# Performance work log

Measured on AMD Instinct MI355X. Metric: run time of the kernel, lower is better.

The kernel has to match this reference:

```python
import jax, jax.numpy as jnp
import numpy as np

B, N, L, E = 8, 2000, 128, 2048  # batch, nodes, local_size+1, ff_hidden_dim
PENALTY = 10.0


def setup_inputs() -> dict:
    key = jax.random.key(0)
    ks = jax.random.split(key, 8)
    dist = jax.random.uniform(ks[0], (B, N, N), jnp.float32) + 1e-3  # positive distances
    theta = jax.random.normal(ks[1], (B, N, N), jnp.float32)
    ins_feature0 = jax.random.normal(ks[2], (B, N, 1), jnp.float32)
    ins_feature1 = jax.random.normal(ks[3], (B, N, 1), jnp.float32)
    d_in = 2 * L + 2
    W1 = jax.random.normal(ks[4], (d_in, E), jnp.float32) * 0.02
    b1 = jnp.zeros((E,), jnp.float32)
    W2 = jax.random.normal(ks[5], (E, L), jnp.float32) * 0.02
    b2 = jnp.zeros((L,), jnp.float32)
    return {"theta": theta, "dist": dist, "ins_feature0": ins_feature0,
            "ins_feature1": ins_feature1, "W1": W1, "b1": b1, "W2": W2, "b2": b2}


def reference(theta, dist, ins_feature0, ins_feature1, W1, b1, W2, b2):
    k = W2.shape[1]  # local_size (L)
    # smallest-k along last dim, sorted ascending (torch.topk largest=False)
    neg_vals, idx = jax.lax.top_k(-dist, k)          # [B,N,L]
    sorted_dist = -neg_vals
    sorted_dist = sorted_dist / jnp.max(sorted_dist, axis=-1, keepdims=True)
    sorted_theta = jnp.take_along_axis(theta, idx, axis=-1)  # [B,N,L]
    x_in = jnp.concatenate([sorted_dist, sorted_theta, ins_feature0, ins_feature1], axis=-1)  # [B,N,2L+2]
    edge_emb = x_in @ W1 + b1                        # [B,N,E] (no nonlinearity, as in source)
    out = edge_emb @ W2 + b2 - sorted_dist           # [B,N,L]
    b_, n_, _ = dist.shape
    bi = jnp.arange(b_)[:, None, None]
    ni = jnp.arange(n_)[None, :, None]
    out_mat = jnp.full(dist.shape, PENALTY, dist.dtype).at[bi, ni, idx].set(out)
    return out_mat
```

## Files before the change

kernel.cpp:

```cpp
#include <hip/hip_runtime.h>
#include <hip/hip_bf16.h>

#define BN 8
#define NN 2000
#define LL 128
#define EE 2048
#define DIN 258
#define KPAD 264
#define NROWS (BN*NN)
#define PENALTY_V 10.0f
#define NBINS 256
#define CANDCAP 256
#define T0 0.092f
#define SPLITK 16
#define ECHUNK (EE/SPLITK)
#define RPB 4
#define AWORDS 5568

__global__ __launch_bounds__(256) void kA1(const float* __restrict__ W1,
                                           const float* __restrict__ b1,
                                           const float* __restrict__ W2,
                                           float* __restrict__ part) {
    __shared__ float As2[8][64];
    const int t = threadIdx.x;
    const int j = t & 127;
    const int half = t >> 7;
    const int rg = blockIdx.x >> 4;
    const int ks = blockIdx.x & 15;
    const int k0 = rg * 8;
    const int ebase = ks * ECHUNK;
    float acc[4] = {0.f, 0.f, 0.f, 0.f};
    for (int ec = ebase; ec < ebase + ECHUNK; ec += 64) {
        #pragma unroll
        for (int q = 0; q < 2; ++q) {
            int linear = q * 256 + t;
            int r8 = linear >> 6;
            int e  = linear & 63;
            int k  = k0 + r8;
            float v;
            if (k < DIN)       v = W1[k * EE + ec + e];
            else if (k == DIN) v = b1[ec + e];
            else               v = 0.0f;
            As2[r8][e] = v;
        }
        __syncthreads();
        #pragma unroll 8
        for (int e = 0; e < 64; ++e) {
            float w = W2[(ec + e) * LL + j];
            #pragma unroll
            for (int rr = 0; rr < 4; ++rr)
                acc[rr] += As2[half * 4 + rr][e] * w;
        }
        __syncthreads();
    }
    #pragma unroll
    for (int rr = 0; rr < 4; ++rr) {
        int k = k0 + half * 4 + rr;
        part[(size_t)ks * (KPAD * LL) + k * LL + j] = acc[rr];
    }
}

__global__ __launch_bounds__(256) void kA2(const float* __restrict__ part,
                                           const float* __restrict__ b2,
                                           float* __restrict__ Wc,
                                           float* __restrict__ bc) {
    const int i = blockIdx.x * 256 + threadIdx.x;
    float s = 0.f;
    #pragma unroll
    for (int q = 0; q < SPLITK; ++q) s += part[(size_t)q * (KPAD * LL) + i];
    const int k = i >> 7;
    const int j = i & 127;
    if (k == DIN)      { bc[j] = s + b2[j]; Wc[i] = 0.f; }
    else if (k > DIN)  { Wc[i] = 0.f; }
    else               { Wc[i] = s; }
}

__global__ __launch_bounds__(256) void kF(const float* __restrict__ dist,
                                          const float* __restrict__ theta,
                                          const float* __restrict__ f0,
                                          const float* __restrict__ f1,
                                          const float* __restrict__ Wc,
                                          const float* __restrict__ bc,
                                          float* __restrict__ out) {
    __shared__ __align__(16) unsigned int arena[AWORDS];
    const int t = threadIdx.x;
    const int lane = t & 63;
    const int w = t >> 6;
    const int row = blockIdx.x * RPB + w;

    unsigned int* hist = &arena[w * 1000];
    unsigned long long* cand = (unsigned long long*)&arena[w * 1000 + 256];
    float* xv = (float*)&arena[4000 + w * 264];
    int* oidx = (int*)&arena[5056 + w * 128];

    {
        uint4 z4 = {0u, 0u, 0u, 0u};
        *(uint4*)&hist[lane * 4] = z4;
        unsigned long long f1v = ~0ULL;
        #pragma unroll
        for (int q = 0; q < CANDCAP / 64; ++q) cand[lane + q * 64] = f1v;
    }

    unsigned int v[32];
    const int nv = (lane < 52) ? 32 : 28;
    {
        const uint4* drow4 = (const uint4*)(dist + (size_t)row * NN);
        #pragma unroll
        for (int q = 0; q < 8; ++q) {
            int qi = q * 64 + lane;
            if (qi < NN / 4) {
                uint4 a = drow4[qi];
                v[4 * q]     = a.x;
                v[4 * q + 1] = a.y;
                v[4 * q + 2] = a.z;
                v[4 * q + 3] = a.w;
            }
        }
    }

    float T = T0;
    unsigned int qm = 0u;
    #pragma unroll
    for (int k = 0; k < 32; ++k)
        if (k < nv && __uint_as_float(v[k]) <= T) qm |= (1u << k);
    int cnt = __builtin_popcount(qm);
    #pragma unroll
    for (int d = 1; d < 64; d <<= 1) cnt += __shfl_xor(cnt, d);

    if (cnt < LL || cnt > CANDCAP) {
        unsigned int lmax = 0u;
        #pragma unroll
        for (int k = 0; k < 32; ++k) if (k < nv) lmax = max(lmax, v[k]);
        #pragma unroll
        for (int d = 1; d < 64; d <<= 1) lmax = max(lmax, (unsigned int)__shfl_xor((int)lmax, d));
        float lo = 0.0f, hi = __uint_as_float(lmax);
        if (cnt < LL) lo = T; else hi = T;
        for (int it = 0; it < 32; ++it) {
            T = 0.5f * (lo + hi);
            unsigned int m = 0u;
            #pragma unroll
            for (int k = 0; k < 32; ++k)
                if (k < nv && __uint_as_float(v[k]) <= T) m |= (1u << k);
            int c = __builtin_popcount(m);
            #pragma unroll
            for (int d = 1; d < 64; d <<= 1) c += __shfl_xor(c, d);
            qm = m;
            if (c >= LL && c <= CANDCAP) break;
            if (c < LL) lo = T; else hi = T;
        }
    }
    const float scale2 = (float)(NBINS - 1) / T;

    #pragma unroll
    for (int k = 0; k < 32; ++k) {
        if ((qm >> k) & 1u) {
            float f = __uint_as_float(v[k]);
            int b = (int)(f * scale2);
            b = b > NBINS - 1 ? NBINS - 1 : b;
            atomicAdd(&hist[b], 1u);
        }
    }

    {
        uint4* h4 = (uint4*)&hist[lane * 4];
        uint4 a0 = *h4;
        unsigned int c[4] = {a0.x, a0.y, a0.z, a0.w};
        unsigned int loc[4], run = 0;
        #pragma unroll
        for (int k = 0; k < 4; ++k) { loc[k] = run; run += c[k]; }
        unsigned int inc = run;
        #pragma unroll
        for (int d = 1; d < 64; d <<= 1) {
            unsigned int o = (unsigned int)__shfl_up((int)inc, d);
            if (lane >= d) inc += o;
        }
        const unsigned int excl = inc - run;
        uint4 s0 = {excl + loc[0], excl + loc[1], excl + loc[2], excl + loc[3]};
        *h4 = s0;
    }

    #pragma unroll
    for (int k = 0; k < 32; ++k) {
        if ((qm >> k) & 1u) {
            unsigned int bits = v[k];
            float f = __uint_as_float(bits);
            int b = (int)(f * scale2);
            b = b > NBINS - 1 ? NBINS - 1 : b;
            unsigned int old = atomicAdd(&hist[b], 0x10000u);
            unsigned int slot = (old & 0xFFFFu) + (old >> 16);
            unsigned int idx = (unsigned int)((k >> 2) * 256 + lane * 4 + (k & 3));
            if (slot < (unsigned int)CANDCAP)
                cand[slot] = ((unsigned long long)bits << 32) | idx;
        }
    }

    {
        unsigned long long key_s[CANDCAP / 64];
        float th_s[CANDCAP / 64];
        #pragma unroll
        for (int s = 0; s < CANDCAP / 64; ++s) key_s[s] = cand[lane + s * 64];
        #pragma unroll
        for (int s = 0; s < CANDCAP / 64; ++s)
            if (key_s[s] != ~0ULL)
                th_s[s] = theta[(size_t)row * NN + (unsigned int)key_s[s]];
        #pragma unroll
        for (int s = 0; s < CANDCAP / 64; ++s) {
            unsigned long long key = key_s[s];
            if (key != ~0ULL) {
                unsigned int bits = (unsigned int)(key >> 32);
                unsigned int idx  = (unsigned int)key;
                float f = __uint_as_float(bits);
                int b = (int)(f * scale2);
                b = b > NBINS - 1 ? NBINS - 1 : b;
                unsigned int word = hist[b];
                unsigned int start = word & 0xFFFFu;
                unsigned int end = start + (word >> 16);
                if (end > (unsigned int)CANDCAP) end = (unsigned int)CANDCAP;
                unsigned int r = start;
                for (unsigned int j = start; j < end; ++j) r += (cand[j] < key);
                if (r < (unsigned int)LL) {
                    xv[r] = f;
                    xv[LL + r] = th_s[s];
                    oidx[r] = (int)idx;
                }
            }
        }
    }

    {
        const float rdm = 1.0f / xv[LL - 1];
        xv[lane] *= rdm;
        xv[lane + 64] *= rdm;
        if (lane == 0) {
            xv[256] = f0[row];
            xv[257] = f1[row];
            #pragma unroll
            for (int z = DIN; z < KPAD; ++z) xv[z] = 0.0f;
        }
    }

    __syncthreads();

    const int j = t & 127;
    const int rp = t >> 7;
    const float* x0 = (const float*)&arena[4000 + (2 * rp) * 264];
    const float* x1 = (const float*)&arena[4000 + (2 * rp + 1) * 264];
    float acc0 = bc[j] - x0[j];
    float acc1 = bc[j] - x1[j];
    #pragma unroll 2
    for (int k = 0; k < KPAD; k += 8) {
        float w0 = Wc[(k + 0) * LL + j];
        float w1 = Wc[(k + 1) * LL + j];
        float w2 = Wc[(k + 2) * LL + j];
        float w3 = Wc[(k + 3) * LL + j];
        float w4 = Wc[(k + 4) * LL + j];
        float w5 = Wc[(k + 5) * LL + j];
        float w6 = Wc[(k + 6) * LL + j];
        float w7 = Wc[(k + 7) * LL + j];
        float4 xa0 = *(const float4*)&x0[k];
        float4 xa1 = *(const float4*)&x0[k + 4];
        float4 xb0 = *(const float4*)&x1[k];
        float4 xb1 = *(const float4*)&x1[k + 4];
        acc0 += xa0.x * w0; acc1 += xb0.x * w0;
        acc0 += xa0.y * w1; acc1 += xb0.y * w1;
        acc0 += xa0.z * w2; acc1 += xb0.z * w2;
        acc0 += xa0.w * w3; acc1 += xb0.w * w3;
        acc0 += xa1.x * w4; acc1 += xb1.x * w4;
        acc0 += xa1.y * w5; acc1 += xb1.y * w5;
        acc0 += xa1.z * w6; acc1 += xb1.z * w6;
        acc0 += xa1.w * w7; acc1 += xb1.w * w7;
    }
    const int oi0 = ((const int*)&arena[5056 + (2 * rp) * 128])[j];
    const int oi1 = ((const int*)&arena[5056 + (2 * rp + 1) * 128])[j];

    float* rowbuf = (float*)arena;
    const float4 pen4 = {PENALTY_V, PENALTY_V, PENALTY_V, PENALTY_V};
    #pragma unroll
    for (int p = 0; p < 2; ++p) {
        __syncthreads();
        for (int i = t; i < 1000; i += 256) ((float4*)rowbuf)[i] = pen4;
        __syncthreads();
        if (rp == p) {
            rowbuf[oi0] = acc0;
            rowbuf[NN + oi1] = acc1;
        }
        __syncthreads();
        float4* o4 = (float4*)(out + ((size_t)blockIdx.x * RPB + 2 * p) * NN);
        for (int i = t; i < 1000; i += 256) o4[i] = ((const float4*)rowbuf)[i];
    }
}

extern "C" void kernel_launch(void* const* d_in, const int* in_sizes, int n_in,
                              void* d_out, int out_size, void* d_ws, size_t ws_size,
                              hipStream_t stream) {
    const float* theta = (const float*)d_in[0];
    const float* dist  = (const float*)d_in[1];
    const float* f0    = (const float*)d_in[2];
    const float* f1    = (const float*)d_in[3];
    const float* W1    = (const float*)d_in[4];
    const float* b1    = (const float*)d_in[5];
    const float* W2    = (const float*)d_in[6];
    const float* b2    = (const float*)d_in[7];
    float* out = (float*)d_out;

    char* ws = (char*)d_ws;
    float* Wc   = (float*)ws;
    float* bc   = (float*)(ws + 135168);
    float* part = (float*)(ws + 135680);

    kA1<<<33 * SPLITK, 256, 0, stream>>>(W1, b1, W2, part);
    kA2<<<(KPAD * LL) / 256, 256, 0, stream>>>(part, b2, Wc, bc);
    kF<<<NROWS / RPB, 256, 0, stream>>>(dist, theta, f0, f1, Wc, bc, out);
}
```

Baseline: 120.1 us.

## Split top-k selection into block-per-row candidate pass and rank-by-count pass

The fused kernel becomes three kernels. A cursor-zeroing kernel runs first. A block-per-row pass then thresholds dist at T0 and appends candidates to a global buffer through a wave scan and an atomic cursor. A final kernel ranks those candidates by brute-force counting comparisons, with no histogram, and falls back to the old bisection and histogram path only when the count is out of range. This spreads the dist scan over more threads to raise memory parallelism, at the cost of extra launches and a global candidate buffer round trip. The candidate buffer reuses the workspace region used by part, which is safe because kA2 consumes part before kPA overwrites it.

```diff
diff --git a/kernel.cpp b/kernel.cpp
--- a/kernel.cpp
+++ b/kernel.cpp
@@ -9,12 +9,12 @@
 #define KPAD 264
 #define NROWS (BN*NN)
 #define PENALTY_V 10.0f
-#define NBINS 256
 #define CANDCAP 256
 #define T0 0.092f
 #define SPLITK 16
 #define ECHUNK (EE/SPLITK)
 #define RPB 4
+#define NBINS 256
 #define AWORDS 5568
 
 __global__ __launch_bounds__(256) void kA1(const float* __restrict__ W1,
@@ -75,153 +75,228 @@
     else               { Wc[i] = s; }
 }
 
-__global__ __launch_bounds__(256) void kF(const float* __restrict__ dist,
-                                          const float* __restrict__ theta,
-                                          const float* __restrict__ f0,
-                                          const float* __restrict__ f1,
-                                          const float* __restrict__ Wc,
-                                          const float* __restrict__ bc,
-                                          float* __restrict__ out) {
+__global__ __launch_bounds__(256) void kZ(unsigned int* __restrict__ cursor) {
+    int i = blockIdx.x * 256 + threadIdx.x;
+    if (i < NROWS) cursor[i] = 0u;
+}
+
+__global__ __launch_bounds__(256) void kPA(const float* __restrict__ dist,
+                                           unsigned long long* __restrict__ candg,
+                                           unsigned int* __restrict__ cursor) {
+    const int t = threadIdx.x;
+    const int lane = t & 63;
+    const int row = blockIdx.x;
+    unsigned int v[8];
+    unsigned int mask8 = 0u;
+    int cnt_l = 0;
+    if (t < 250) {
+        const uint4* d4 = (const uint4*)(dist + (size_t)row * NN);
+        uint4 a = d4[2 * t], b = d4[2 * t + 1];
+        v[0] = a.x; v[1] = a.y; v[2] = a.z; v[3] = a.w;
+        v[4] = b.x; v[5] = b.y; v[6] = b.z; v[7] = b.w;
+        #pragma unroll
+        for (int e = 0; e < 8; ++e)
+            if (__uint_as_float(v[e]) <= T0) mask8 |= (1u << e);
+        cnt_l = __builtin_popcount(mask8);
+    }
+    int inc = cnt_l;
+    #pragma unroll
+    for (int d = 1; d < 64; d <<= 1) {
+        int o = __shfl_up(inc, d);
+        if (lane >= d) inc += o;
+    }
+    const int excl = inc - cnt_l;
+    unsigned int ret = 0u;
+    if (lane == 63) ret = atomicAdd(&cursor[row], (unsigned int)inc);
+    const unsigned int base = (unsigned int)__shfl((int)ret, 63);
+    unsigned int off = base + (unsigned int)excl;
+    #pragma unroll
+    for (int e = 0; e < 8; ++e) {
+        if ((mask8 >> e) & 1u) {
+            if (off < (unsigned int)CANDCAP)
+                candg[(size_t)row * CANDCAP + off] =
+                    ((unsigned long long)v[e] << 32) | (unsigned int)(8 * t + e);
+            ++off;
+        }
+    }
+}
+
+__global__ __launch_bounds__(256) void kPB(const float* __restrict__ dist,
+                                           const float* __restrict__ theta,
+                                           const float* __restrict__ f0,
+                                           const float* __restrict__ f1,
+                                           const unsigned long long* __restrict__ candg,
+                                           const unsigned int* __restrict__ cursor,
+                                           const float* __restrict__ Wc,
+                                           const float* __restrict__ bc,
+                                           float* __restrict__ out) {
     __shared__ __align__(16) unsigned int arena[AWORDS];
     const int t = threadIdx.x;
     const int lane = t & 63;
     const int w = t >> 6;
     const int row = blockIdx.x * RPB + w;
 
-    unsigned int* hist = &arena[w * 1000];
-    unsigned long long* cand = (unsigned long long*)&arena[w * 1000 + 256];
     float* xv = (float*)&arena[4000 + w * 264];
     int* oidx = (int*)&arena[5056 + w * 128];
-
-    {
-        uint4 z4 = {0u, 0u, 0u, 0u};
-        *(uint4*)&hist[lane * 4] = z4;
-        unsigned long long f1v = ~0ULL;
+    const unsigned int cnt = cursor[row];
+
+    if (cnt >= (unsigned int)LL && cnt <= (unsigned int)CANDCAP) {
+        unsigned long long* keys = (unsigned long long*)&arena[w * 1000];
+        unsigned long long k0v, k1v, k2v, k3v;
+        {
+            const unsigned long long* cg = candg + (size_t)row * CANDCAP;
+            k0v = (lane        < (int)cnt) ? cg[lane]        : ~0ULL;
+            k1v = (lane + 64   < (int)cnt) ? cg[lane + 64]   : ~0ULL;
+            k2v = (lane + 128  < (int)cnt) ? cg[lane + 128]  : ~0ULL;
+            k3v = (lane + 192  < (int)cnt) ? cg[lane + 192]  : ~0ULL;
+            keys[lane] = k0v; keys[lane + 64] = k1v;
+            keys[lane + 128] = k2v; keys[lane + 192] = k3v;
+        }
+        float th0 = 0.f, th1 = 0.f, th2 = 0.f, th3 = 0.f;
+        if (k0v != ~0ULL) th0 = theta[(size_t)row * NN + (unsigned int)k0v];
+        if (k1v != ~0ULL) th1 = theta[(size_t)row * NN + (unsigned int)k1v];
+        if (k2v != ~0ULL) th2 = theta[(size_t)row * NN + (unsigned int)k2v];
+        if (k3v != ~0ULL) th3 = theta[(size_t)row * NN + (unsigned int)k3v];
+        unsigned int r0 = 0, r1 = 0, r2 = 0, r3 = 0;
+        for (unsigned int j = 0; j < cnt; ++j) {
+            const unsigned long long kj = keys[j];
+            r0 += (kj < k0v); r1 += (kj < k1v);
+            r2 += (kj < k2v); r3 += (kj < k3v);
+        }
+        if (k0v != ~0ULL && r0 < (unsigned int)LL) {
+            xv[r0] = __uint_as_float((unsigned int)(k0v >> 32));
+            xv[LL + r0] = th0; oidx[r0] = (int)(unsigned int)k0v;
+        }
+        if (k1v != ~0ULL && r1 < (unsigned int)LL) {
+            xv[r1] = __uint_as_float((unsigned int)(k1v >> 32));
+            xv[LL + r1] = th1; oidx[r1] = (int)(unsigned int)k1v;
+        }
+        if (k2v != ~0ULL && r2 < (unsigned int)LL) {
+            xv[r2] = __uint_as_float((unsigned int)(k2v >> 32));
+            xv[LL + r2] = th2; oidx[r2] = (int)(unsigned int)k2v;
+        }
+        if (k3v != ~0ULL && r3 < (unsigned int)LL) {
+            xv[r3] = __uint_as_float((unsigned int)(k3v >> 32));
+            xv[LL + r3] = th3; oidx[r3] = (int)(unsigned int)k3v;
+        }
+    } else {
+        unsigned int* hist = &arena[w * 1000];
+        unsigned long long* cand = (unsigned long long*)&arena[w * 1000 + 256];
+        {
+            uint4 z4 = {0u, 0u, 0u, 0u};
+            *(uint4*)&hist[lane * 4] = z4;
+            unsigned long long f1v = ~0ULL;
+            #pragma unroll
+            for (int q = 0; q < CANDCAP / 64; ++q) cand[lane + q * 64] = f1v;
+        }
+        unsigned int v[32];
+        const int nv = (lane < 52) ? 32 : 28;
+        {
+            const uint4* drow4 = (const uint4*)(dist + (size_t)row * NN);
+            #pragma unroll
+            for (int q = 0; q < 8; ++q) {
+                int qi = q * 64 + lane;
+                if (qi < NN / 4) {
+                    uint4 a = drow4[qi];
+                    v[4 * q] = a.x; v[4 * q + 1] = a.y;
+                    v[4 * q + 2] = a.z; v[4 * q + 3] = a.w;
+                }
+            }
+        }
+        float T = T0;
+        unsigned int qm = 0u;
+        {
+            unsigned int lmax = 0u;
+            #pragma unroll
+            for (int k = 0; k < 32; ++k) if (k < nv) lmax = max(lmax, v[k]);
+            #pragma unroll
+            for (int d = 1; d < 64; d <<= 1) lmax = max(lmax, (unsigned int)__shfl_xor((int)lmax, d));
+            float lo = 0.0f, hi = __uint_as_float(lmax);
+            if (cnt < (unsigned int)LL) lo = T; else hi = T;
+            for (int it = 0; it < 32; ++it) {
+                T = 0.5f * (lo + hi);
+                unsigned int m = 0u;
+                #pragma unroll
+                for (int k = 0; k < 32; ++k)
+                    if (k < nv && __uint_as_float(v[k]) <= T) m |= (1u << k);
+                int c = __builtin_popcount(m);
+                #pragma unroll
+                for (int d = 1; d < 64; d <<= 1) c += __shfl_xor(c, d);
+                qm = m;
+                if (c >= LL && c <= CANDCAP) break;
+                if (c < LL) lo = T; else hi = T;
+            }
+        }
+        const float scale2 = (float)(NBINS - 1) / T;
         #pragma unroll
-        for (int q = 0; q < CANDCAP / 64; ++q) cand[lane + q * 64] = f1v;
-    }
-
-    unsigned int v[32];
-    const int nv = (lane < 52) ? 32 : 28;
-    {
-        const uint4* drow4 = (const uint4*)(dist + (size_t)row * NN);
+        for (int k = 0; k < 32; ++k) {
+            if ((qm >> k) & 1u) {
+                float f = __uint_as_float(v[k]);
+                int b = (int)(f * scale2);
+                b = b > NBINS - 1 ? NBINS - 1 : b;
+                atomicAdd(&hist[b], 1u);
+            }
+        }
+        {
+            uint4* h4 = (uint4*)&hist[lane * 4];
+            uint4 a0 = *h4;
+            unsigned int c[4] = {a0.x, a0.y, a0.z, a0.w};
+            unsigned int loc[4], run = 0;
+            #pragma unroll
+            for (int k = 0; k < 4; ++k) { loc[k] = run; run += c[k]; }
+            unsigned int inc = run;
+            #pragma unroll
+            for (int d = 1; d < 64; d <<= 1) {
+                unsigned int o = (unsigned int)__shfl_up((int)inc, d);
+                if (lane >= d) inc += o;
+            }
+            const unsigned int excl = inc - run;
+            uint4 s0 = {excl + loc[0], excl + loc[1], excl + loc[2], excl + loc[3]};
+            *h4 = s0;
+        }
         #pragma unroll
-        for (int q = 0; q < 8; ++q) {
-            int qi = q * 64 + lane;
-            if (qi < NN / 4) {
-                uint4 a = drow4[qi];
-                v[4 * q]     = a.x;
-                v[4 * q + 1] = a.y;
-                v[4 * q + 2] = a.z;
-                v[4 * q + 3] = a.w;
-            }
-        }
-    }
-
-    float T = T0;
-    unsigned int qm = 0u;
-    #pragma unroll
-    for (int k = 0; k < 32; ++k)
-        if (k < nv && __uint_as_float(v[k]) <= T) qm |= (1u << k);
-    int cnt = __builtin_popcount(qm);
-    #pragma unroll
-    for (int d = 1; d < 64; d <<= 1) cnt += __shfl_xor(cnt, d);
-
-    if (cnt < LL || cnt > CANDCAP) {
-        unsigned int lmax = 0u;
-        #pragma unroll
-        for (int k = 0; k < 32; ++k) if (k < nv) lmax = max(lmax, v[k]);
-        #pragma unroll
-        for (int d = 1; d < 64; d <<= 1) lmax = max(lmax, (unsigned int)__shfl_xor((int)lmax, d));
-        float lo = 0.0f, hi = __uint_as_float(lmax);
-        if (cnt < LL) lo = T; else hi = T;
-        for (int it = 0; it < 32; ++it) {
-            T = 0.5f * (lo + hi);
-            unsigned int m = 0u;
-            #pragma unroll
-            for (int k = 0; k < 32; ++k)
-                if (k < nv && __uint_as_float(v[k]) <= T) m |= (1u << k);
-            int c = __builtin_popcount(m);
-            #pragma unroll
-            for (int d = 1; d < 64; d <<= 1) c += __shfl_xor(c, d);
-            qm = m;
-            if (c >= LL && c <= CANDCAP) break;
-            if (c < LL) lo = T; else hi = T;
-        }
-    }
-    const float scale2 = (float)(NBINS - 1) / T;
-
-    #pragma unroll
-    for (int k = 0; k < 32; ++k) {
-        if ((qm >> k) & 1u) {
-            float f = __uint_as_float(v[k]);
-            int b = (int)(f * scale2);
-            b = b > NBINS - 1 ? NBINS - 1 : b;
-            atomicAdd(&hist[b], 1u);
-        }
-    }
-
-    {
-        uint4* h4 = (uint4*)&hist[lane * 4];
-        uint4 a0 = *h4;
-        unsigned int c[4] = {a0.x, a0.y, a0.z, a0.w};
-        unsigned int loc[4], run = 0;
-        #pragma unroll
-        for (int k = 0; k < 4; ++k) { loc[k] = run; run += c[k]; }
-        unsigned int inc = run;
-        #pragma unroll
-        for (int d = 1; d < 64; d <<= 1) {
-            unsigned int o = (unsigned int)__shfl_up((int)inc, d);
-            if (lane >= d) inc += o;
-        }
-        const unsigned int excl = inc - run;
-        uint4 s0 = {excl + loc[0], excl + loc[1], excl + loc[2], excl + loc[3]};
-        *h4 = s0;
-    }
-
-    #pragma unroll
-    for (int k = 0; k < 32; ++k) {
-        if ((qm >> k) & 1u) {
-            unsigned int bits = v[k];
-            float f = __uint_as_float(bits);
-            int b = (int)(f * scale2);
-            b = b > NBINS - 1 ? NBINS - 1 : b;
-            unsigned int old = atomicAdd(&hist[b], 0x10000u);
-            unsigned int slot = (old & 0xFFFFu) + (old >> 16);
-            unsigned int idx = (unsigned int)((k >> 2) * 256 + lane * 4 + (k & 3));
-            if (slot < (unsigned int)CANDCAP)
-                cand[slot] = ((unsigned long long)bits << 32) | idx;
-        }
-    }
-
-    {
-        unsigned long long key_s[CANDCAP / 64];
-        float th_s[CANDCAP / 64];
-        #pragma unroll
-        for (int s = 0; s < CANDCAP / 64; ++s) key_s[s] = cand[lane + s * 64];
-        #pragma unroll
-        for (int s = 0; s < CANDCAP / 64; ++s)
-            if (key_s[s] != ~0ULL)
-                th_s[s] = theta[(size_t)row * NN + (unsigned int)key_s[s]];
-        #pragma unroll
-        for (int s = 0; s < CANDCAP / 64; ++s) {
-            unsigned long long key = key_s[s];
-            if (key != ~0ULL) {
-                unsigned int bits = (unsigned int)(key >> 32);
-                unsigned int idx  = (unsigned int)key;
+        for (int k = 0; k < 32; ++k) {
+            if ((qm >> k) & 1u) {
+                unsigned int bits = v[k];
                 float f = __uint_as_float(bits);
                 int b = (int)(f * scale2);
                 b = b > NBINS - 1 ? NBINS - 1 : b;
-                unsigned int word = hist[b];
-                unsigned int start = word & 0xFFFFu;
-                unsigned int end = start + (word >> 16);
-                if (end > (unsigned int)CANDCAP) end = (unsigned int)CANDCAP;
-                unsigned int r = start;
-                for (unsigned int j = start; j < end; ++j) r += (cand[j] < key);
-                if (r < (unsigned int)LL) {
-                    xv[r] = f;
-                    xv[LL + r] = th_s[s];
-                    oidx[r] = (int)idx;
+                unsigned int old = atomicAdd(&hist[b], 0x10000u);
+                unsigned int slot = (old & 0xFFFFu) + (old >> 16);
+                unsigned int idx = (unsigned int)((k >> 2) * 256 + lane * 4 + (k & 3));
+                if (slot < (unsigned int)CANDCAP)
+                    cand[slot] = ((unsigned long long)bits << 32) | idx;
+            }
+        }
+        {
+            unsigned long long key_s[CANDCAP / 64];
+            float th_s[CANDCAP / 64];
+            #pragma unroll
+            for (int s = 0; s < CANDCAP / 64; ++s) key_s[s] = cand[lane + s * 64];
+            #pragma unroll
+            for (int s = 0; s < CANDCAP / 64; ++s)
+                if (key_s[s] != ~0ULL)
+                    th_s[s] = theta[(size_t)row * NN + (unsigned int)key_s[s]];
+            #pragma unroll
+            for (int s = 0; s < CANDCAP / 64; ++s) {
+                unsigned long long key = key_s[s];
+                if (key != ~0ULL) {
+                    unsigned int bits = (unsigned int)(key >> 32);
+                    unsigned int idx  = (unsigned int)key;
+                    float f = __uint_as_float(bits);
+                    int b = (int)(f * scale2);
+                    b = b > NBINS - 1 ? NBINS - 1 : b;
+                    unsigned int word = hist[b];
+                    unsigned int start = word & 0xFFFFu;
+                    unsigned int end = start + (word >> 16);
+                    if (end > (unsigned int)CANDCAP) end = (unsigned int)CANDCAP;
+                    unsigned int r = start;
+                    for (unsigned int j = start; j < end; ++j) r += (cand[j] < key);
+                    if (r < (unsigned int)LL) {
+                        xv[r] = f;
+                        xv[LL + r] = th_s[s];
+                        oidx[r] = (int)idx;
+                    }
                 }
             }
         }
@@ -307,8 +382,12 @@
     float* Wc   = (float*)ws;
     float* bc   = (float*)(ws + 135168);
     float* part = (float*)(ws + 135680);
+    unsigned long long* candg = (unsigned long long*)(ws + 135680);
+    unsigned int* cursor = (unsigned int*)(ws + 135680 + 32768000);
 
     kA1<<<33 * SPLITK, 256, 0, stream>>>(W1, b1, W2, part);
     kA2<<<(KPAD * LL) / 256, 256, 0, stream>>>(part, b2, Wc, bc);
-    kF<<<NROWS / RPB, 256, 0, stream>>>(dist, theta, f0, f1, Wc, bc, out);
-}
+    kZ<<<(NROWS + 255) / 256, 256, 0, stream>>>(cursor);
+    kPA<<<NROWS, 256, 0, stream>>>(dist, candg, cursor);
+    kPB<<<NROWS / RPB, 256, 0, stream>>>(dist, theta, f0, f1, candg, cursor, Wc, bc, out);
+}
```

New measurement: 138.0 us. +14.9%, slower.
